# Kernel optimization log

Hardware: AMD Instinct MI355X
Metric: run time of the kernel (lower is better)

Reference implementation:

```python
import jax, jax.numpy as jnp
import numpy as np

N = 50000
NEG_SLOPE = 0.2


def add_self_loops(edge_index, n):
    loops = jnp.arange(n, dtype=edge_index.dtype)
    return jnp.concatenate([edge_index, jnp.stack([loops, loops])], axis=1)


def gat_layer(x, edge_index, W, a_src, a_dst, b, heads, ch):
    # x: [N, F_in], W: [F_in, heads*ch], a_src/a_dst: [heads, ch], b: [heads*ch]
    n = x.shape[0]
    src, dst = edge_index[0], edge_index[1]
    h = (x @ W).reshape(n, heads, ch)                      # [N, H, C]
    alpha_src = jnp.sum(h * a_src, axis=-1)                # [N, H]
    alpha_dst = jnp.sum(h * a_dst, axis=-1)                # [N, H]
    e = jax.nn.leaky_relu(alpha_src[src] + alpha_dst[dst], NEG_SLOPE)  # [E, H]
    # segment softmax over incoming edges of each destination node
    m = jax.ops.segment_max(e, dst, num_segments=n)        # [N, H]
    ex = jnp.exp(e - m[dst])                               # [E, H]
    denom = jax.ops.segment_sum(ex, dst, num_segments=n)   # [N, H]
    alpha = ex / (denom[dst] + 1e-16)                      # [E, H]
    msg = h[src] * alpha[:, :, None]                       # [E, H, C]
    out = jax.ops.segment_sum(msg, dst, num_segments=n)    # [N, H, C]
    return out.reshape(n, heads * ch) + b


def setup_inputs() -> dict:
    key = jax.random.key(0)
    ks = jax.random.split(key, 12)
    input_dim, hidden_dim, output_dim, heads = 128, 32, 64, 4
    E = 1600000
    x = jax.random.normal(ks[0], (N, input_dim), dtype=jnp.float32)
    edge_index = jax.random.randint(ks[1], (2, E), 0, N, dtype=jnp.int64)
    s1 = 1.0 / np.sqrt(input_dim)
    s2 = 1.0 / np.sqrt(hidden_dim * heads)
    W1 = jax.random.uniform(ks[2], (input_dim, heads * hidden_dim), jnp.float32, -s1, s1)
    a_src1 = jax.random.uniform(ks[3], (heads, hidden_dim), jnp.float32, -s1, s1)
    a_dst1 = jax.random.uniform(ks[4], (heads, hidden_dim), jnp.float32, -s1, s1)
    b1 = jnp.zeros((heads * hidden_dim,), jnp.float32)
    W2 = jax.random.uniform(ks[5], (heads * hidden_dim, output_dim), jnp.float32, -s2, s2)
    a_src2 = jax.random.uniform(ks[6], (1, output_dim), jnp.float32, -s2, s2)
    a_dst2 = jax.random.uniform(ks[7], (1, output_dim), jnp.float32, -s2, s2)
    b2 = jnp.zeros((output_dim,), jnp.float32)
    return {"x": x, "edge_index": edge_index,
            "W1": W1, "a_src1": a_src1, "a_dst1": a_dst1, "b1": b1,
            "W2": W2, "a_src2": a_src2, "a_dst2": a_dst2, "b2": b2}


def reference(x, edge_index, W1, a_src1, a_dst1, b1, W2, a_src2, a_dst2, b2):
    n = x.shape[0]
    ei = add_self_loops(edge_index, n)
    h = gat_layer(x, ei, W1, a_src1, a_dst1, b1, heads=4, ch=32)
    h = jax.nn.relu(h)
    out = gat_layer(h, ei, W2, a_src2, a_dst2, b2, heads=1, ch=64)
    return out
```

## Files before the change

### kernel.cpp

```cpp
#include <hip/hip_runtime.h>
#include <hip/hip_bf16.h>
#include <hip/hip_fp16.h>


#define LRELU_SLOPE 0.2f
#define NBMAX 200
#define NBLK  512
#define BCAP  16384
#define CAPIMG 16384

typedef _Float16 f16x8 __attribute__((ext_vector_type(8)));
typedef _Float16 f16x4 __attribute__((ext_vector_type(4)));
typedef float f32x4 __attribute__((ext_vector_type(4)));


__global__ __launch_bounds__(256) void hist_kernel(const int* __restrict__ ei_dst,
                                                   int* __restrict__ hist, int E, int chunk) {
    __shared__ int h[NBMAX];
    int t = threadIdx.x;
    for (int i = t; i < NBMAX; i += 256) h[i] = 0;
    __syncthreads();
    int begin = blockIdx.x * chunk;
    int endE = min(E, begin + chunk);
    for (int e = begin + t; e < endE; e += 256) atomicAdd(&h[ei_dst[e] >> 8], 1);
    __syncthreads();
    for (int i = t; i < NBMAX; i += 256) hist[i * NBLK + blockIdx.x] = h[i];
}

__global__ __launch_bounds__(512) void bucket_scan_kernel(int* __restrict__ hist,
                                                          int* __restrict__ gfill) {
    __shared__ int buf[2][NBLK];
    int b = blockIdx.x, t = threadIdx.x;
    buf[0][t] = hist[b * NBLK + t];
    __syncthreads();
    int pi = 0;
#pragma unroll
    for (int off = 1; off < NBLK; off <<= 1) {
        int v = buf[pi][t];
        if (t >= off) v += buf[pi][t - off];
        buf[pi ^ 1][t] = v;
        __syncthreads();
        pi ^= 1;
    }
    hist[b * NBLK + t] = (t == 0) ? 0 : buf[pi][t - 1];
    if (t == 0) gfill[b] = buf[pi][NBLK - 1];
}

__global__ __launch_bounds__(256) void scatter2_kernel(const int* __restrict__ ei_src,
                                                       const int* __restrict__ ei_dst,
                                                       const int* __restrict__ hist,
                                                       unsigned int* __restrict__ records,
                                                       int E, int chunk) {
    __shared__ int base[NBMAX];
    __shared__ int lcnt[NBMAX];
    int t = threadIdx.x;
    for (int i = t; i < NBMAX; i += 256) {
        base[i] = hist[i * NBLK + blockIdx.x];
        lcnt[i] = 0;
    }
    __syncthreads();
    int begin = blockIdx.x * chunk;
    int endE = min(E, begin + chunk);
    for (int e = begin + t; e < endE; e += 256) {
        int s = ei_src[e], d = ei_dst[e];
        int bkt = d >> 8;
        unsigned int rec = (unsigned int)d | ((unsigned int)s << 16);
        int r = atomicAdd(&lcnt[bkt], 1);
        records[(size_t)bkt * BCAP + base[bkt] + r] = rec;
    }
}

__global__ __launch_bounds__(256) void deg_kernel(const unsigned int* __restrict__ records,
                                                  const int* __restrict__ gfill,
                                                  int* __restrict__ deg, int N) {
    __shared__ int cnt[256];
    int t = threadIdx.x, b = blockIdx.x;
    cnt[t] = 1;
    __syncthreads();
    int c = gfill[b];
    const unsigned int* r = records + (size_t)b * BCAP;
    for (int i = t; i < c; i += 256) atomicAdd(&cnt[r[i] & 255], 1);
    __syncthreads();
    int gi = (b << 8) + t;
    if (gi < N) deg[gi] = cnt[t];
}

__global__ __launch_bounds__(256) void scan_blocksums_kernel(const int* __restrict__ gfill,
                                                             int* __restrict__ bsums,
                                                             int* __restrict__ row_ptr,
                                                             int nblocks, int n, int total) {
    __shared__ int buf[2][256];
    int t = threadIdx.x;
    int v0 = 0;
    if (t < nblocks) v0 = gfill[t] + min(256, n - (t << 8));
    buf[0][t] = v0;
    __syncthreads();
    int pi = 0;
#pragma unroll
    for (int off = 1; off < 256; off <<= 1) {
        int v = buf[pi][t];
        if (t >= off) v += buf[pi][t - off];
        buf[pi ^ 1][t] = v;
        __syncthreads();
        pi ^= 1;
    }
    if (t < nblocks) bsums[t] = (t == 0) ? 0 : buf[pi][t - 1];
    if (t == 0) row_ptr[n] = total;
}

__global__ __launch_bounds__(256) void scan_down_kernel(const int* __restrict__ deg,
                                                        const int* __restrict__ blockSums,
                                                        int* __restrict__ row_ptr, int n) {
    __shared__ int buf[2][256];
    int t = threadIdx.x;
    int i = blockIdx.x * 256 + t;
    int d = (i < n) ? deg[i] : 0;
    buf[0][t] = d;
    __syncthreads();
    int pi = 0;
#pragma unroll
    for (int off = 1; off < 256; off <<= 1) {
        int v = buf[pi][t];
        if (t >= off) v += buf[pi][t - off];
        buf[pi ^ 1][t] = v;
        __syncthreads();
        pi ^= 1;
    }
    if (i < n) row_ptr[i] = blockSums[blockIdx.x] + buf[pi][t] - d;
}

__global__ __launch_bounds__(256) void csr_scatter_kernel(const unsigned int* __restrict__ records,
                                                          const int* __restrict__ gfill,
                                                          const int* __restrict__ row_ptr,
                                                          unsigned short* __restrict__ col,
                                                          int N) {
    __shared__ unsigned short img[CAPIMG];
    __shared__ int lfill[256];
    int t = threadIdx.x, b = blockIdx.x;
    int bBase = b << 8;
    int bEnd = min(bBase + 256, N);
    int rbase = row_ptr[bBase];
    int size = row_ptr[bEnd] - rbase;
    bool lds = (size <= CAPIMG);
    int gi = bBase + t;
    if (gi < bEnd) {
        int rp = row_ptr[gi];
        int local = rp - rbase;
        lfill[t] = local + 1;
        if (lds) img[local] = (unsigned short)gi;
        else col[rp] = (unsigned short)gi;
    }
    __syncthreads();
    int c = gfill[b];
    const unsigned int* r = records + (size_t)b * BCAP;
    for (int i = t; i < c; i += 256) {
        unsigned int rec = r[i];
        int d8 = rec & 255;
        unsigned short s = (unsigned short)(rec >> 16);
        int p = atomicAdd(&lfill[d8], 1);
        if (lds) img[p] = s;
        else col[rbase + p] = s;
    }
    __syncthreads();
    if (lds) {
        for (int i = t; i < size; i += 256) col[rbase + i] = img[i];
    }
}


__global__ __launch_bounds__(256) void gemm1_mfma_kernel(const float* __restrict__ X,
                                                         const float* __restrict__ W,
                                                         __half* __restrict__ outh,
                                                         const float* __restrict__ a_src,
                                                         const float* __restrict__ a_dst,
                                                         float* __restrict__ as_out,
                                                         float* __restrict__ ad_out, int nrows) {
    constexpr int KP = 136;
    __shared__ _Float16 wlds[128 * KP];
    int t = threadIdx.x;
    int wv = t >> 6, lane = t & 63;
    int quad = lane >> 4, m16 = lane & 15;
    for (int i = t; i < 4096; i += 256) {
        int k = i >> 5;
        int n0 = (i & 31) << 2;
        float4 v = *(const float4*)(W + k * 128 + n0);
        wlds[(n0 + 0) * KP + k] = (_Float16)v.x;
        wlds[(n0 + 1) * KP + k] = (_Float16)v.y;
        wlds[(n0 + 2) * KP + k] = (_Float16)v.z;
        wlds[(n0 + 3) * KP + k] = (_Float16)v.w;
    }
    __syncthreads();

    int row = blockIdx.x * 64 + wv * 16 + m16;
    int rowC = min(row, nrows - 1);
    const float* xp = X + (size_t)rowC * 128;

    f32x4 acc[8];
#pragma unroll
    for (int nt = 0; nt < 8; ++nt) acc[nt] = (f32x4)0.f;

    for (int kt = 0; kt < 128; kt += 32) {
        float4 v0 = *(const float4*)(xp + kt + quad * 8);
        float4 v1 = *(const float4*)(xp + kt + quad * 8 + 4);
        f16x8 af;
        af[0] = (_Float16)v0.x; af[1] = (_Float16)v0.y;
        af[2] = (_Float16)v0.z; af[3] = (_Float16)v0.w;
        af[4] = (_Float16)v1.x; af[5] = (_Float16)v1.y;
        af[6] = (_Float16)v1.z; af[7] = (_Float16)v1.w;
#pragma unroll
        for (int nt = 0; nt < 8; ++nt) {
            f16x8 bf = *(const f16x8*)(&wlds[(nt * 16 + m16) * KP + kt + quad * 8]);
            acc[nt] = __builtin_amdgcn_mfma_f32_16x16x32_f16(af, bf, acc[nt], 0, 0, 0);
        }
    }

    float aS[8], aD[8];
#pragma unroll
    for (int nt = 0; nt < 8; ++nt) {
        aS[nt] = a_src[nt * 16 + m16];
        aD[nt] = a_dst[nt * 16 + m16];
    }
    int rowBaseW = blockIdx.x * 64 + wv * 16;
#pragma unroll
    for (int r = 0; r < 4; ++r) {
        int orow = rowBaseW + quad * 4 + r;
        bool ov = orow < nrows;
        if (ov) {
#pragma unroll
            for (int nt = 0; nt < 8; ++nt)
                outh[(size_t)orow * 128 + nt * 16 + m16] = __float2half(acc[nt][r]);
        }
#pragma unroll
        for (int h = 0; h < 4; ++h) {
            float ss = acc[2 * h][r] * aS[2 * h] + acc[2 * h + 1][r] * aS[2 * h + 1];
            float dd = acc[2 * h][r] * aD[2 * h] + acc[2 * h + 1][r] * aD[2 * h + 1];
#pragma unroll
            for (int o = 1; o < 16; o <<= 1) {
                ss += __shfl_xor(ss, o, 64);
                dd += __shfl_xor(dd, o, 64);
            }
            if (ov && m16 == h) {
                as_out[orow * 4 + h] = ss;
                ad_out[orow * 4 + h] = dd;
            }
        }
    }
}


__global__ __launch_bounds__(256) void gemm2_mfma_kernel(const __half* __restrict__ Xh,
                                                         const float* __restrict__ W,
                                                         __half* __restrict__ outh,
                                                         const float* __restrict__ a_src,
                                                         const float* __restrict__ a_dst,
                                                         float* __restrict__ as_out,
                                                         float* __restrict__ ad_out, int nrows) {
    constexpr int KP = 136;
    __shared__ _Float16 wlds[64 * KP];
    int t = threadIdx.x;
    int wv = t >> 6, lane = t & 63;
    int quad = lane >> 4, m16 = lane & 15;
    for (int i = t; i < 2048; i += 256) {
        int k = i >> 4;
        int n0 = (i & 15) << 2;
        float4 v = *(const float4*)(W + k * 64 + n0);
        wlds[(n0 + 0) * KP + k] = (_Float16)v.x;
        wlds[(n0 + 1) * KP + k] = (_Float16)v.y;
        wlds[(n0 + 2) * KP + k] = (_Float16)v.z;
        wlds[(n0 + 3) * KP + k] = (_Float16)v.w;
    }
    __syncthreads();

    int row = blockIdx.x * 64 + wv * 16 + m16;
    int rowC = min(row, nrows - 1);
    const _Float16* xp = (const _Float16*)Xh + (size_t)rowC * 128;

    f32x4 acc[4];
#pragma unroll
    for (int nt = 0; nt < 4; ++nt) acc[nt] = (f32x4)0.f;

    for (int kt = 0; kt < 128; kt += 32) {
        f16x8 af = *(const f16x8*)(xp + kt + quad * 8);
#pragma unroll
        for (int nt = 0; nt < 4; ++nt) {
            f16x8 bf = *(const f16x8*)(&wlds[(nt * 16 + m16) * KP + kt + quad * 8]);
            acc[nt] = __builtin_amdgcn_mfma_f32_16x16x32_f16(af, bf, acc[nt], 0, 0, 0);
        }
    }

    float aS[4], aD[4];
#pragma unroll
    for (int nt = 0; nt < 4; ++nt) {
        aS[nt] = a_src[nt * 16 + m16];
        aD[nt] = a_dst[nt * 16 + m16];
    }
    int rowBaseW = blockIdx.x * 64 + wv * 16;
#pragma unroll
    for (int r = 0; r < 4; ++r) {
        int orow = rowBaseW + quad * 4 + r;
        bool ov = orow < nrows;
        if (ov) {
#pragma unroll
            for (int nt = 0; nt < 4; ++nt)
                outh[(size_t)orow * 64 + nt * 16 + m16] = __float2half(acc[nt][r]);
        }
        float ss = 0.f, dd = 0.f;
#pragma unroll
        for (int nt = 0; nt < 4; ++nt) {
            ss = fmaf(acc[nt][r], aS[nt], ss);
            dd = fmaf(acc[nt][r], aD[nt], dd);
        }
#pragma unroll
        for (int o = 1; o < 16; o <<= 1) {
            ss += __shfl_xor(ss, o, 64);
            dd += __shfl_xor(dd, o, 64);
        }
        if (ov && m16 == 0) {
            as_out[orow] = ss;
            ad_out[orow] = dd;
        }
    }
}


__global__ __launch_bounds__(256) void agg1_kernel(const __half* __restrict__ h1h,
                                                   const float* __restrict__ asrc,
                                                   const float* __restrict__ adst,
                                                   const int* __restrict__ row_ptr,
                                                   const unsigned short* __restrict__ col,
                                                   const float* __restrict__ b1,
                                                   __half* __restrict__ out, int n) {
    int wave = threadIdx.x >> 6;
    int lane = threadIdx.x & 63;
    int node = blockIdx.x * 4 + wave;
    if (node >= n) return;
    int half = lane >> 5;
    int m = lane & 31;
    int head = m >> 3;
    const char* __restrict__ h1c = (const char*)h1h;
    const char* __restrict__ asc = (const char*)asrc;
    unsigned moff = (unsigned)m << 3;
    unsigned aoff = (unsigned)head << 2;
    float ad = adst[node * 4 + head];
    int start = row_ptr[node], end = row_ptr[node + 1];
    float a0c = 0.f, a1c = 0.f, a2c = 0.f, a3c = 0.f, s = 0.f;
    for (int base = start; base < end; base += 64) {
        int cnt = min(64, end - base);
        int idx = base + lane;
        int myS = (idx < end) ? (int)col[idx] : 0;
        for (int j = 0; j < cnt; j += 12) {
            int jj[6];
            int sv[6];
#pragma unroll
            for (int k = 0; k < 6; ++k) {
                jj[k] = j + 2 * k + half;
                sv[k] = __shfl(myS, jj[k], 64);
            }
            f16x4 v[6];
            float as[6];
#pragma unroll
            for (int k = 0; k < 6; ++k) {
                v[k]  = *(const f16x4*)(h1c + ((((unsigned)sv[k]) << 8) | moff));
                as[k] = *(const float*)(asc + ((((unsigned)sv[k]) << 4) | aoff));
            }
#pragma unroll
            for (int k = 0; k < 6; ++k) {
                float e = as[k] + ad;
                e = fmaxf(e, LRELU_SLOPE * e);
                float p = (jj[k] < cnt) ? __expf(e) : 0.f;
                a0c = fmaf(p, (float)v[k][0], a0c);
                a1c = fmaf(p, (float)v[k][1], a1c);
                a2c = fmaf(p, (float)v[k][2], a2c);
                a3c = fmaf(p, (float)v[k][3], a3c);
                s += p;
            }
        }
    }
    a0c += __shfl_xor(a0c, 32, 64);
    a1c += __shfl_xor(a1c, 32, 64);
    a2c += __shfl_xor(a2c, 32, 64);
    a3c += __shfl_xor(a3c, 32, 64);
    s   += __shfl_xor(s, 32, 64);
    if (half == 0) {
        float inv = 1.f / (s + 1e-16f);
        float4 bb = ((const float4*)b1)[m];
        f16x4 o;
        o[0] = (_Float16)fmaxf(fmaf(a0c, inv, bb.x), 0.f);
        o[1] = (_Float16)fmaxf(fmaf(a1c, inv, bb.y), 0.f);
        o[2] = (_Float16)fmaxf(fmaf(a2c, inv, bb.z), 0.f);
        o[3] = (_Float16)fmaxf(fmaf(a3c, inv, bb.w), 0.f);
        ((f16x4*)out)[node * 32 + m] = o;
    }
}

__global__ __launch_bounds__(256) void agg2_kernel(const __half* __restrict__ h2bh,
                                                   const float* __restrict__ asrc,
                                                   const float* __restrict__ adst,
                                                   const int* __restrict__ row_ptr,
                                                   const unsigned short* __restrict__ col,
                                                   const float* __restrict__ b2,
                                                   float* __restrict__ out, int n) {
    int wave = threadIdx.x >> 6;
    int lane = threadIdx.x & 63;
    int node = blockIdx.x * 4 + wave;
    if (node >= n) return;
    int q = lane >> 4;
    int m = lane & 15;
    const char* __restrict__ h2c = (const char*)h2bh;
    const char* __restrict__ asc = (const char*)asrc;
    unsigned moff = (unsigned)m << 3;
    float ad = adst[node];
    int start = row_ptr[node], end = row_ptr[node + 1];
    float a0c = 0.f, a1c = 0.f, a2c = 0.f, a3c = 0.f, s = 0.f;
    for (int base = start; base < end; base += 64) {
        int cnt = min(64, end - base);
        int idx = base + lane;
        int myS = (idx < end) ? (int)col[idx] : 0;
        for (int j = 0; j < cnt; j += 12) {
            int jj[3];
            int sv[3];
#pragma unroll
            for (int k = 0; k < 3; ++k) {
                jj[k] = j + 4 * k + q;
                sv[k] = __shfl(myS, jj[k], 64);
            }
            f16x4 v[3];
            float as[3];
#pragma unroll
            for (int k = 0; k < 3; ++k) {
                v[k]  = *(const f16x4*)(h2c + ((((unsigned)sv[k]) << 7) | moff));
                as[k] = *(const float*)(asc + (((unsigned)sv[k]) << 2));
            }
#pragma unroll
            for (int k = 0; k < 3; ++k) {
                float e = as[k] + ad;
                e = fmaxf(e, LRELU_SLOPE * e);
                float p = (jj[k] < cnt) ? __expf(e) : 0.f;
                a0c = fmaf(p, (float)v[k][0], a0c);
                a1c = fmaf(p, (float)v[k][1], a1c);
                a2c = fmaf(p, (float)v[k][2], a2c);
                a3c = fmaf(p, (float)v[k][3], a3c);
                s += p;
            }
        }
    }
#pragma unroll
    for (int o = 16; o <= 32; o <<= 1) {
        a0c += __shfl_xor(a0c, o, 64);
        a1c += __shfl_xor(a1c, o, 64);
        a2c += __shfl_xor(a2c, o, 64);
        a3c += __shfl_xor(a3c, o, 64);
        s   += __shfl_xor(s, o, 64);
    }
    if (lane < 16) {
        float inv = 1.f / (s + 1e-16f);
        float4 bb = ((const float4*)b2)[m];
        float4 o;
        o.x = fmaf(a0c, inv, bb.x);
        o.y = fmaf(a1c, inv, bb.y);
        o.z = fmaf(a2c, inv, bb.z);
        o.w = fmaf(a3c, inv, bb.w);
        ((float4*)(out + (size_t)node * 64))[m] = o;
    }
}


extern "C" void kernel_launch(void* const* d_in, const int* in_sizes, int n_in,
                              void* d_out, int out_size, void* d_ws, size_t ws_size,
                              hipStream_t stream) {
    const float* x      = (const float*)d_in[0];
    const int*   ei     = (const int*)d_in[1];
    const float* W1     = (const float*)d_in[2];
    const float* a_src1 = (const float*)d_in[3];
    const float* a_dst1 = (const float*)d_in[4];
    const float* b1     = (const float*)d_in[5];
    const float* W2     = (const float*)d_in[6];
    const float* a_src2 = (const float*)d_in[7];
    const float* a_dst2 = (const float*)d_in[8];
    const float* b2     = (const float*)d_in[9];
    float* out = (float*)d_out;

    const int N = in_sizes[0] / 128;
    const int E = in_sizes[1] / 2;
    const int total = E + N;
    const int nBuckets = (N + 255) >> 8;

    char* ws = (char*)d_ws;
    size_t off = 0;
    auto alloc = [&](size_t bytes) {
        void* p = ws + off;
        off += (bytes + 255) & ~(size_t)255;
        return p;
    };
    float* regionA = (float*)alloc((size_t)N * 128 * 4);
    __half* h1h   = (__half*)alloc((size_t)N * 128 * 2);
    __half* h2bh  = (__half*)alloc((size_t)N * 64 * 2);
    float* asrc1  = (float*)alloc((size_t)N * 4 * 4);
    float* adst1  = (float*)alloc((size_t)N * 4 * 4);
    float* asrc2  = (float*)alloc((size_t)N * 4);
    float* adst2  = (float*)alloc((size_t)N * 4);
    int*   deg    = (int*)alloc((size_t)N * 4);
    int*   row_ptr= (int*)alloc((size_t)(N + 1) * 4);
    int*   gfill  = (int*)alloc((size_t)nBuckets * 4);
    int*   bsums  = (int*)alloc((size_t)nBuckets * 4);
    unsigned short* col = (unsigned short*)alloc((size_t)total * 2);

    unsigned int* records = (unsigned int*)regionA;
    int* hist = (int*)(regionA + (size_t)NBMAX * BCAP);
    __half* h2in = (__half*)regionA;
    (void)ws_size; (void)n_in; (void)out_size;

    const int* ei_src = ei;
    const int* ei_dst = ei + E;

    const int chunk = (E + NBLK - 1) / NBLK;
    hist_kernel<<<NBLK, 256, 0, stream>>>(ei_dst, hist, E, chunk);
    bucket_scan_kernel<<<nBuckets, NBLK, 0, stream>>>(hist, gfill);
    scatter2_kernel<<<NBLK, 256, 0, stream>>>(ei_src, ei_dst, hist, records, E, chunk);
    deg_kernel<<<nBuckets, 256, 0, stream>>>(records, gfill, deg, N);
    scan_blocksums_kernel<<<1, 256, 0, stream>>>(gfill, bsums, row_ptr, nBuckets, N, total);
    scan_down_kernel<<<nBuckets, 256, 0, stream>>>(deg, bsums, row_ptr, N);
    csr_scatter_kernel<<<nBuckets, 256, 0, stream>>>(records, gfill, row_ptr, col, N);

    gemm1_mfma_kernel<<<(N + 63) / 64, 256, 0, stream>>>(x, W1, h1h, a_src1, a_dst1,
                                                         asrc1, adst1, N);
    agg1_kernel<<<(N + 3) / 4, 256, 0, stream>>>(h1h, asrc1, adst1,
                                                 row_ptr, col, b1, h2in, N);

    gemm2_mfma_kernel<<<(N + 63) / 64, 256, 0, stream>>>(h2in, W2, h2bh, a_src2, a_dst2,
                                                         asrc2, adst2, N);
    agg2_kernel<<<(N + 3) / 4, 256, 0, stream>>>(h2bh, asrc2, adst2,
                                                 row_ptr, col, b2, out, N);
}
```

Baseline: 247.0 us.

## Split layer-1 aggregation across eight channel slices per node

Layer-1 aggregation is re-partitioned so each node is handled by eight blocks, each covering a 16-channel slice (half a head). Within a wave, 16 edge slots times 4 sub-lanes process 32 edges per iteration, with a shuffle reduction at the end. The aim is more parallelism and shorter per-wave edge loops, giving better latency hiding on gathers. In exchange, col indices and attention scores are re-read eight times per node, and exp is recomputed redundantly for each slice.

```diff
diff --git a/kernel.cpp b/kernel.cpp
--- a/kernel.cpp
+++ b/kernel.cpp
@@ -330,66 +330,63 @@
                                                    const unsigned short* __restrict__ col,
                                                    const float* __restrict__ b1,
                                                    __half* __restrict__ out, int n) {
+    unsigned bid = blockIdx.x;
+    int slice = (int)(bid & 7u);
+    int ng = (int)(bid >> 3);
     int wave = threadIdx.x >> 6;
     int lane = threadIdx.x & 63;
-    int node = blockIdx.x * 4 + wave;
+    int node = ng * 4 + wave;
     if (node >= n) return;
-    int half = lane >> 5;
-    int m = lane & 31;
-    int head = m >> 3;
+    int eslot = lane >> 2;
+    int sub = lane & 3;
+    int head = slice >> 1;
     const char* __restrict__ h1c = (const char*)h1h;
     const char* __restrict__ asc = (const char*)asrc;
-    unsigned moff = (unsigned)m << 3;
+    unsigned coff = ((unsigned)slice << 5) | ((unsigned)sub << 3);
     unsigned aoff = (unsigned)head << 2;
     float ad = adst[node * 4 + head];
     int start = row_ptr[node], end = row_ptr[node + 1];
-    float a0c = 0.f, a1c = 0.f, a2c = 0.f, a3c = 0.f, s = 0.f;
-    for (int base = start; base < end; base += 64) {
-        int cnt = min(64, end - base);
-        int idx = base + lane;
-        int myS = (idx < end) ? (int)col[idx] : 0;
-        for (int j = 0; j < cnt; j += 12) {
-            int jj[6];
-            int sv[6];
-#pragma unroll
-            for (int k = 0; k < 6; ++k) {
-                jj[k] = j + 2 * k + half;
-                sv[k] = __shfl(myS, jj[k], 64);
-            }
-            f16x4 v[6];
-            float as[6];
-#pragma unroll
-            for (int k = 0; k < 6; ++k) {
-                v[k]  = *(const f16x4*)(h1c + ((((unsigned)sv[k]) << 8) | moff));
-                as[k] = *(const float*)(asc + ((((unsigned)sv[k]) << 4) | aoff));
-            }
-#pragma unroll
-            for (int k = 0; k < 6; ++k) {
-                float e = as[k] + ad;
-                e = fmaxf(e, LRELU_SLOPE * e);
-                float p = (jj[k] < cnt) ? __expf(e) : 0.f;
-                a0c = fmaf(p, (float)v[k][0], a0c);
-                a1c = fmaf(p, (float)v[k][1], a1c);
-                a2c = fmaf(p, (float)v[k][2], a2c);
-                a3c = fmaf(p, (float)v[k][3], a3c);
-                s += p;
-            }
-        }
-    }
-    a0c += __shfl_xor(a0c, 32, 64);
-    a1c += __shfl_xor(a1c, 32, 64);
-    a2c += __shfl_xor(a2c, 32, 64);
-    a3c += __shfl_xor(a3c, 32, 64);
-    s   += __shfl_xor(s, 32, 64);
-    if (half == 0) {
+    float a0 = 0.f, a1 = 0.f, a2 = 0.f, a3 = 0.f, s = 0.f;
+    for (int base = start; base < end; base += 32) {
+        int iA = base + eslot;
+        int iB = iA + 16;
+        int sA = (int)col[min(iA, end - 1)];
+        int sB = (int)col[min(iB, end - 1)];
+        f16x4 vA = *(const f16x4*)(h1c + ((((unsigned)sA) << 8) | coff));
+        f16x4 vB = *(const f16x4*)(h1c + ((((unsigned)sB) << 8) | coff));
+        float eA = *(const float*)(asc + ((((unsigned)sA) << 4) | aoff)) + ad;
+        float eB = *(const float*)(asc + ((((unsigned)sB) << 4) | aoff)) + ad;
+        eA = fmaxf(eA, LRELU_SLOPE * eA);
+        eB = fmaxf(eB, LRELU_SLOPE * eB);
+        float pA = (iA < end) ? __expf(eA) : 0.f;
+        float pB = (iB < end) ? __expf(eB) : 0.f;
+        a0 = fmaf(pA, (float)vA[0], a0);
+        a1 = fmaf(pA, (float)vA[1], a1);
+        a2 = fmaf(pA, (float)vA[2], a2);
+        a3 = fmaf(pA, (float)vA[3], a3);
+        a0 = fmaf(pB, (float)vB[0], a0);
+        a1 = fmaf(pB, (float)vB[1], a1);
+        a2 = fmaf(pB, (float)vB[2], a2);
+        a3 = fmaf(pB, (float)vB[3], a3);
+        s += pA + pB;
+    }
+#pragma unroll
+    for (int o = 4; o < 64; o <<= 1) {
+        a0 += __shfl_xor(a0, o, 64);
+        a1 += __shfl_xor(a1, o, 64);
+        a2 += __shfl_xor(a2, o, 64);
+        a3 += __shfl_xor(a3, o, 64);
+        s  += __shfl_xor(s, o, 64);
+    }
+    if (lane < 4) {
         float inv = 1.f / (s + 1e-16f);
-        float4 bb = ((const float4*)b1)[m];
+        float4 bb = ((const float4*)b1)[slice * 4 + sub];
         f16x4 o;
-        o[0] = (_Float16)fmaxf(fmaf(a0c, inv, bb.x), 0.f);
-        o[1] = (_Float16)fmaxf(fmaf(a1c, inv, bb.y), 0.f);
-        o[2] = (_Float16)fmaxf(fmaf(a2c, inv, bb.z), 0.f);
-        o[3] = (_Float16)fmaxf(fmaf(a3c, inv, bb.w), 0.f);
-        ((f16x4*)out)[node * 32 + m] = o;
+        o[0] = (_Float16)fmaxf(fmaf(a0, inv, bb.x), 0.f);
+        o[1] = (_Float16)fmaxf(fmaf(a1, inv, bb.y), 0.f);
+        o[2] = (_Float16)fmaxf(fmaf(a2, inv, bb.z), 0.f);
+        o[3] = (_Float16)fmaxf(fmaf(a3, inv, bb.w), 0.f);
+        ((f16x4*)out)[node * 32 + slice * 4 + sub] = o;
     }
 }
 
@@ -524,8 +521,8 @@
 
     gemm1_mfma_kernel<<<(N + 63) / 64, 256, 0, stream>>>(x, W1, h1h, a_src1, a_dst1,
                                                          asrc1, adst1, N);
-    agg1_kernel<<<(N + 3) / 4, 256, 0, stream>>>(h1h, asrc1, adst1,
-                                                 row_ptr, col, b1, h2in, N);
+    agg1_kernel<<<((N + 3) / 4) * 8, 256, 0, stream>>>(h1h, asrc1, adst1,
+                                                       row_ptr, col, b1, h2in, N);
 
     gemm2_mfma_kernel<<<(N + 63) / 64, 256, 0, stream>>>(h2in, W2, h2bh, a_src2, a_dst2,
                                                          asrc2, adst2, N);
```

Result: slower. 390.5 us (+58.1%).

## Fuse CSR degree count, scan and scatter; widen agg2 per-lane channel loads

Applied to the files above, without the earlier changes.

Merges the degree-count, per-bucket scan and CSR scatter kernels into one kernel that computes per-node degrees and local offsets in shared memory, using the bucket sums directly. This drops two kernel launches and the global deg/row_ptr round trip. Separately, agg2 now has each lane handle 8 fp16 channels for 8 edge slots, processing 16 edges per iteration, in place of 4 channels over 4 edge slots. This cuts shuffles and branches per edge, at the cost of more reduction shuffles at the end and more wasted lanes on low-degree nodes.

```diff
diff --git a/kernel.cpp b/kernel.cpp
--- a/kernel.cpp
+++ b/kernel.cpp
@@ -70,21 +70,6 @@
     }
 }
 
-__global__ __launch_bounds__(256) void deg_kernel(const unsigned int* __restrict__ records,
-                                                  const int* __restrict__ gfill,
-                                                  int* __restrict__ deg, int N) {
-    __shared__ int cnt[256];
-    int t = threadIdx.x, b = blockIdx.x;
-    cnt[t] = 1;
-    __syncthreads();
-    int c = gfill[b];
-    const unsigned int* r = records + (size_t)b * BCAP;
-    for (int i = t; i < c; i += 256) atomicAdd(&cnt[r[i] & 255], 1);
-    __syncthreads();
-    int gi = (b << 8) + t;
-    if (gi < N) deg[gi] = cnt[t];
-}
-
 __global__ __launch_bounds__(256) void scan_blocksums_kernel(const int* __restrict__ gfill,
                                                              int* __restrict__ bsums,
                                                              int* __restrict__ row_ptr,
@@ -108,51 +93,46 @@
     if (t == 0) row_ptr[n] = total;
 }
 
-__global__ __launch_bounds__(256) void scan_down_kernel(const int* __restrict__ deg,
-                                                        const int* __restrict__ blockSums,
-                                                        int* __restrict__ row_ptr, int n) {
-    __shared__ int buf[2][256];
-    int t = threadIdx.x;
-    int i = blockIdx.x * 256 + t;
-    int d = (i < n) ? deg[i] : 0;
-    buf[0][t] = d;
-    __syncthreads();
-    int pi = 0;
-#pragma unroll
-    for (int off = 1; off < 256; off <<= 1) {
-        int v = buf[pi][t];
-        if (t >= off) v += buf[pi][t - off];
-        buf[pi ^ 1][t] = v;
-        __syncthreads();
-        pi ^= 1;
-    }
-    if (i < n) row_ptr[i] = blockSums[blockIdx.x] + buf[pi][t] - d;
-}
-
-__global__ __launch_bounds__(256) void csr_scatter_kernel(const unsigned int* __restrict__ records,
-                                                          const int* __restrict__ gfill,
-                                                          const int* __restrict__ row_ptr,
-                                                          unsigned short* __restrict__ col,
-                                                          int N) {
+__global__ __launch_bounds__(256) void csr_fused_kernel(const unsigned int* __restrict__ records,
+                                                        const int* __restrict__ gfill,
+                                                        const int* __restrict__ bsums,
+                                                        int* __restrict__ row_ptr,
+                                                        unsigned short* __restrict__ col,
+                                                        int N) {
     __shared__ unsigned short img[CAPIMG];
+    __shared__ int cnt[2][256];
     __shared__ int lfill[256];
     int t = threadIdx.x, b = blockIdx.x;
     int bBase = b << 8;
     int bEnd = min(bBase + 256, N);
-    int rbase = row_ptr[bBase];
-    int size = row_ptr[bEnd] - rbase;
+    int rbase = bsums[b];
+    int c = gfill[b];
+    int size = c + (bEnd - bBase);
     bool lds = (size <= CAPIMG);
+    const unsigned int* r = records + (size_t)b * BCAP;
     int gi = bBase + t;
+    cnt[0][t] = (gi < bEnd) ? 1 : 0;
+    __syncthreads();
+    for (int i = t; i < c; i += 256) atomicAdd(&cnt[0][r[i] & 255], 1);
+    __syncthreads();
+    int d = cnt[0][t];
+    int pi = 0;
+#pragma unroll
+    for (int off = 1; off < 256; off <<= 1) {
+        int v = cnt[pi][t];
+        if (t >= off) v += cnt[pi][t - off];
+        cnt[pi ^ 1][t] = v;
+        __syncthreads();
+        pi ^= 1;
+    }
+    int local = cnt[pi][t] - d;
     if (gi < bEnd) {
-        int rp = row_ptr[gi];
-        int local = rp - rbase;
+        row_ptr[gi] = rbase + local;
         lfill[t] = local + 1;
         if (lds) img[local] = (unsigned short)gi;
-        else col[rp] = (unsigned short)gi;
-    }
-    __syncthreads();
-    int c = gfill[b];
-    const unsigned int* r = records + (size_t)b * BCAP;
+        else col[rbase + local] = (unsigned short)gi;
+    }
+    __syncthreads();
     for (int i = t; i < c; i += 256) {
         unsigned int rec = r[i];
         int d8 = rec & 255;
@@ -404,63 +384,56 @@
     int lane = threadIdx.x & 63;
     int node = blockIdx.x * 4 + wave;
     if (node >= n) return;
-    int q = lane >> 4;
-    int m = lane & 15;
+    int eslot = lane >> 3;
+    int sub = lane & 7;
     const char* __restrict__ h2c = (const char*)h2bh;
-    const char* __restrict__ asc = (const char*)asrc;
-    unsigned moff = (unsigned)m << 3;
+    unsigned coff = (unsigned)sub << 4;
     float ad = adst[node];
     int start = row_ptr[node], end = row_ptr[node + 1];
-    float a0c = 0.f, a1c = 0.f, a2c = 0.f, a3c = 0.f, s = 0.f;
-    for (int base = start; base < end; base += 64) {
-        int cnt = min(64, end - base);
-        int idx = base + lane;
-        int myS = (idx < end) ? (int)col[idx] : 0;
-        for (int j = 0; j < cnt; j += 12) {
-            int jj[3];
-            int sv[3];
-#pragma unroll
-            for (int k = 0; k < 3; ++k) {
-                jj[k] = j + 4 * k + q;
-                sv[k] = __shfl(myS, jj[k], 64);
-            }
-            f16x4 v[3];
-            float as[3];
-#pragma unroll
-            for (int k = 0; k < 3; ++k) {
-                v[k]  = *(const f16x4*)(h2c + ((((unsigned)sv[k]) << 7) | moff));
-                as[k] = *(const float*)(asc + (((unsigned)sv[k]) << 2));
-            }
-#pragma unroll
-            for (int k = 0; k < 3; ++k) {
-                float e = as[k] + ad;
-                e = fmaxf(e, LRELU_SLOPE * e);
-                float p = (jj[k] < cnt) ? __expf(e) : 0.f;
-                a0c = fmaf(p, (float)v[k][0], a0c);
-                a1c = fmaf(p, (float)v[k][1], a1c);
-                a2c = fmaf(p, (float)v[k][2], a2c);
-                a3c = fmaf(p, (float)v[k][3], a3c);
-                s += p;
-            }
-        }
-    }
-#pragma unroll
-    for (int o = 16; o <= 32; o <<= 1) {
-        a0c += __shfl_xor(a0c, o, 64);
-        a1c += __shfl_xor(a1c, o, 64);
-        a2c += __shfl_xor(a2c, o, 64);
-        a3c += __shfl_xor(a3c, o, 64);
-        s   += __shfl_xor(s, o, 64);
-    }
-    if (lane < 16) {
+    float acc[8];
+#pragma unroll
+    for (int c = 0; c < 8; ++c) acc[c] = 0.f;
+    float s = 0.f;
+    for (int base = start; base < end; base += 16) {
+        int iA = base + eslot;
+        int iB = iA + 8;
+        int sA = (int)col[min(iA, end - 1)];
+        int sB = (int)col[min(iB, end - 1)];
+        f16x8 vA = *(const f16x8*)(h2c + ((((unsigned)sA) << 7) | coff));
+        f16x8 vB = *(const f16x8*)(h2c + ((((unsigned)sB) << 7) | coff));
+        float eA = asrc[sA] + ad;
+        float eB = asrc[sB] + ad;
+        eA = fmaxf(eA, LRELU_SLOPE * eA);
+        eB = fmaxf(eB, LRELU_SLOPE * eB);
+        float pA = (iA < end) ? __expf(eA) : 0.f;
+        float pB = (iB < end) ? __expf(eB) : 0.f;
+#pragma unroll
+        for (int c = 0; c < 8; ++c) acc[c] = fmaf(pA, (float)vA[c], acc[c]);
+#pragma unroll
+        for (int c = 0; c < 8; ++c) acc[c] = fmaf(pB, (float)vB[c], acc[c]);
+        s += pA + pB;
+    }
+#pragma unroll
+    for (int o = 8; o < 64; o <<= 1) {
+#pragma unroll
+        for (int c = 0; c < 8; ++c) acc[c] += __shfl_xor(acc[c], o, 64);
+        s += __shfl_xor(s, o, 64);
+    }
+    if (lane < 8) {
         float inv = 1.f / (s + 1e-16f);
-        float4 bb = ((const float4*)b2)[m];
-        float4 o;
-        o.x = fmaf(a0c, inv, bb.x);
-        o.y = fmaf(a1c, inv, bb.y);
-        o.z = fmaf(a2c, inv, bb.z);
-        o.w = fmaf(a3c, inv, bb.w);
-        ((float4*)(out + (size_t)node * 64))[m] = o;
+        float4 bb0 = ((const float4*)b2)[sub * 2];
+        float4 bb1 = ((const float4*)b2)[sub * 2 + 1];
+        float4 o0, o1;
+        o0.x = fmaf(acc[0], inv, bb0.x);
+        o0.y = fmaf(acc[1], inv, bb0.y);
+        o0.z = fmaf(acc[2], inv, bb0.z);
+        o0.w = fmaf(acc[3], inv, bb0.w);
+        o1.x = fmaf(acc[4], inv, bb1.x);
+        o1.y = fmaf(acc[5], inv, bb1.y);
+        o1.z = fmaf(acc[6], inv, bb1.z);
+        o1.w = fmaf(acc[7], inv, bb1.w);
+        ((float4*)(out + (size_t)node * 64))[sub * 2] = o0;
+        ((float4*)(out + (size_t)node * 64))[sub * 2 + 1] = o1;
     }
 }
 
@@ -499,7 +472,6 @@
     float* adst1  = (float*)alloc((size_t)N * 4 * 4);
     float* asrc2  = (float*)alloc((size_t)N * 4);
     float* adst2  = (float*)alloc((size_t)N * 4);
-    int*   deg    = (int*)alloc((size_t)N * 4);
     int*   row_ptr= (int*)alloc((size_t)(N + 1) * 4);
     int*   gfill  = (int*)alloc((size_t)nBuckets * 4);
     int*   bsums  = (int*)alloc((size_t)nBuckets * 4);
@@ -517,10 +489,8 @@
     hist_kernel<<<NBLK, 256, 0, stream>>>(ei_dst, hist, E, chunk);
     bucket_scan_kernel<<<nBuckets, NBLK, 0, stream>>>(hist, gfill);
     scatter2_kernel<<<NBLK, 256, 0, stream>>>(ei_src, ei_dst, hist, records, E, chunk);
-    deg_kernel<<<nBuckets, 256, 0, stream>>>(records, gfill, deg, N);
     scan_blocksums_kernel<<<1, 256, 0, stream>>>(gfill, bsums, row_ptr, nBuckets, N, total);
-    scan_down_kernel<<<nBuckets, 256, 0, stream>>>(deg, bsums, row_ptr, N);
-    csr_scatter_kernel<<<nBuckets, 256, 0, stream>>>(records, gfill, row_ptr, col, N);
+    csr_fused_kernel<<<nBuckets, 256, 0, stream>>>(records, gfill, bsums, row_ptr, col, N);
 
     gemm1_mfma_kernel<<<(N + 63) / 64, 256, 0, stream>>>(x, W1, h1h, a_src1, a_dst1,
                                                          asrc1, adst1, N);
```

Result: no change. 244.7 us (-1.0%).
